# Kernel tuning notes

Hardware: AMD Instinct MI355X
Metric: run time of the kernel (lower is better)

The kernel has to match this reference:

```python
import jax, jax.numpy as jnp
import numpy as np

B, D, C = 8192, 2048, 1000

def setup_inputs() -> dict:
    key = jax.random.key(0)
    k1, k2, k3 = jax.random.split(key, 3)
    x = jax.random.normal(k1, (B, D), dtype=jnp.float32)
    W = jax.random.normal(k2, (D, C), dtype=jnp.float32) * (1.0 / np.sqrt(D))
    b = jax.random.normal(k3, (C,), dtype=jnp.float32) * 0.01
    return {"x": x, "W": W, "b": b}

def reference(x, W, b):
    # inner classifier: logits out[b, c]
    out = jnp.dot(x, W) + b  # [B, C]
    # leave-one-out logsumexp per class, fused:
    # lse_k = logsumexp(out[:, != k]) = lse_all + log1p(-exp(out_k - lse_all))
    lse = jax.nn.logsumexp(out, axis=1, keepdims=True)  # [B, 1]
    loo = lse + jnp.log1p(-jnp.exp(out - lse))           # [B, C]
    # c_out = -loo; return c_out + out
    return out - loo
```

## Files before the change

### kernel.cpp

```cpp
#include <hip/hip_runtime.h>
#include <hip/hip_bf16.h>
#include <math.h>

#define BDIM 8192
#define DDIM 2048
#define CDIM 1000
#define NPAD 1024
#define BK   64

#define WS_BT_OFFSET  33554432ULL
#define WS_P0_OFFSET  37748736ULL
#define WS_P1_OFFSET  54132736ULL
#define WS_NEED       70516736ULL

typedef __attribute__((ext_vector_type(8))) short short8;
typedef __attribute__((ext_vector_type(4))) float floatx4;

__device__ __forceinline__ unsigned short f2bf(float f) {
    union { float f; unsigned u; } a; a.f = f;
    unsigned u = a.u;
    u = (u + 0x7fff + ((u >> 16) & 1)) >> 16;
    return (unsigned short)u;
}

__device__ __forceinline__ float bf2f(unsigned short h) {
    union { unsigned u; float f; } a; a.u = ((unsigned)h) << 16;
    return a.f;
}

__device__ __forceinline__ void async_copy16(const void* gp, void* lp) {
    __builtin_amdgcn_global_load_lds(
        (const __attribute__((address_space(1))) void*)gp,
        (__attribute__((address_space(3))) void*)lp,
        16, 0, 0);
}

__global__ __launch_bounds__(256) void cvt_kernel(
    const float* __restrict__ x, unsigned short* __restrict__ xb,
    const float* __restrict__ W, unsigned short* __restrict__ Bt)
{
    const int blk = blockIdx.x;
    const int t   = threadIdx.x;
    if (blk < 16384) {
        int i = blk * 256 + t;
        float4 v = ((const float4*)x)[i];
        ushort4 o;
        o.x = f2bf(v.x); o.y = f2bf(v.y); o.z = f2bf(v.z); o.w = f2bf(v.w);
        ((ushort4*)xb)[i] = o;
    } else {
        __shared__ float tile[32][33];
        const int b2 = blk - 16384;
        const int k0 = (b2 & 63) * 32;
        const int n0 = (b2 >> 6) * 32;
        const int tx = t & 31, ty = t >> 5;
        #pragma unroll
        for (int i = 0; i < 4; i++) {
            int k = k0 + ty + i * 8;
            int n = n0 + tx;
            tile[ty + i * 8][tx] = (n < CDIM) ? W[(size_t)k * CDIM + n] : 0.0f;
        }
        __syncthreads();
        #pragma unroll
        for (int i = 0; i < 4; i++) {
            int n = n0 + ty + i * 8;
            int k = k0 + tx;
            Bt[(size_t)n * DDIM + k] = f2bf(tile[tx][ty + i * 8]);
        }
    }
}

template <bool BF16OUT>
__device__ __forceinline__ void gemm_body(
    const unsigned short* __restrict__ A,
    const unsigned short* __restrict__ Bt,
    void* __restrict__ Cv,
    int mBase, int nBase, int kBase, int kIters,
    unsigned short* As, unsigned short* Bs)
{
    const int t    = threadIdx.x;
    const int wave = t >> 6;
    const int lane = t & 63;
    const int wm   = wave & 1;
    const int wn   = wave >> 1;
    const int quad = lane >> 4;
    const int l16  = lane & 15;

    floatx4 acc[4][4] = {};

    const int rowA = t >> 3;
    const int csw  = ((t & 7) ^ (rowA & 7)) * 16;
    const char* Ag = (const char*)A  + ((size_t)(mBase + rowA) * DDIM + kBase) * 2 + csw;
    const char* Bg = (const char*)Bt + ((size_t)(nBase + rowA) * DDIM + kBase) * 2 + csw;
    char* AsDst = (char*)As + t * 16;
    char* BsDst = (char*)Bs + t * 16;

    const int xorb0 = ((0 * 4 + quad) ^ (l16 & 7)) * 8;
    const int xorb1 = ((1 * 4 + quad) ^ (l16 & 7)) * 8;

    for (int kt = 0; kt < kIters * BK; kt += BK) {
        const char* a = Ag + kt * 2;
        const char* b = Bg + kt * 2;
        #pragma unroll
        for (int r = 0; r < 4; r++) {
            async_copy16(a + (size_t)r * 32 * DDIM * 2, AsDst + r * 4096);
            async_copy16(b + (size_t)r * 32 * DDIM * 2, BsDst + r * 4096);
        }
        __syncthreads();

        #pragma unroll
        for (int ks = 0; ks < 2; ks++) {
            const int xorb = ks ? xorb1 : xorb0;
            short8 af[4], bfr[4];
            #pragma unroll
            for (int mi = 0; mi < 4; mi++)
                af[mi] = *(const short8*)(As + (wm * 64 + mi * 16 + l16) * BK + xorb);
            #pragma unroll
            for (int ni = 0; ni < 4; ni++)
                bfr[ni] = *(const short8*)(Bs + (wn * 64 + ni * 16 + l16) * BK + xorb);
            #pragma unroll
            for (int mi = 0; mi < 4; mi++)
                #pragma unroll
                for (int ni = 0; ni < 4; ni++)
                    acc[mi][ni] = __builtin_amdgcn_mfma_f32_16x16x32_bf16(
                        af[mi], bfr[ni], acc[mi][ni], 0, 0, 0);
        }
        __syncthreads();
    }

    #pragma unroll
    for (int mi = 0; mi < 4; mi++) {
        int row0 = mBase + wm * 64 + mi * 16 + quad * 4;
        #pragma unroll
        for (int ni = 0; ni < 4; ni++) {
            int col = nBase + wn * 64 + ni * 16 + l16;
            if (col < CDIM) {
                #pragma unroll
                for (int rg = 0; rg < 4; rg++) {
                    if (BF16OUT)
                        ((unsigned short*)Cv)[(size_t)(row0 + rg) * CDIM + col] =
                            f2bf(acc[mi][ni][rg]);
                    else
                        ((float*)Cv)[(size_t)(row0 + rg) * CDIM + col] = acc[mi][ni][rg];
                }
            }
        }
    }
}

__global__ __launch_bounds__(256, 2) void gemm_single_kernel(
    const unsigned short* __restrict__ A,
    const unsigned short* __restrict__ Bt,
    float* __restrict__ C0)
{
    __shared__ unsigned short As[128 * BK];
    __shared__ unsigned short Bs[128 * BK];

    const int L   = blockIdx.x;
    const int xcd = L & 7;
    const int s   = L >> 3;
    const int m_t = xcd * 8 + (s >> 3);
    const int n_t = s & 7;

    gemm_body<false>(A, Bt, C0, m_t * 128, n_t * 128, 0, DDIM / BK, As, Bs);
}


#define STAGE_A(BUF, EXT, KO)                                                 \
    do {                                                                      \
        _Pragma("unroll")                                                     \
        for (int h = 0; h < 2; h++) {                                         \
            const int row_ = rA0 + (EXT) + h * 128;                           \
            async_copy16(gA + (size_t)row_ * DDIM + (KO),                     \
                         &As[BUF][row_ * BK + c8]);                           \
        }                                                                     \
    } while (0)

#define STAGE_B(BUF, EXT, KO)                                                 \
    do {                                                                      \
        _Pragma("unroll")                                                     \
        for (int h = 0; h < 2; h++) {                                         \
            const int row_ = rB0 + (EXT) + h * 128;                           \
            async_copy16(gB + (size_t)row_ * DDIM + (KO),                     \
                         &Bs[BUF][row_ * BK + c8]);                           \
        }                                                                     \
    } while (0)

#define LOADA(BUF, MQ)                                                        \
    do {                                                                      \
        _Pragma("unroll")                                                     \
        for (int mf = 0; mf < 4; mf++) {                                      \
            const int r_ = (arA + (MQ) * 64 + mf * 16) * BK;                  \
            af[mf][0] = *(const short8*)&As[BUF][r_ + xorb0];                 \
            af[mf][1] = *(const short8*)&As[BUF][r_ + xorb1];                 \
        }                                                                     \
    } while (0)

#define LOADB(BUF, NQ, BF)                                                    \
    do {                                                                      \
        _Pragma("unroll")                                                     \
        for (int nf = 0; nf < 2; nf++) {                                      \
            const int r_ = (arB + (NQ) * 32 + nf * 16) * BK;                  \
            BF[nf][0] = *(const short8*)&Bs[BUF][r_ + xorb0];                 \
            BF[nf][1] = *(const short8*)&Bs[BUF][r_ + xorb1];                 \
        }                                                                     \
    } while (0)

#define MMAC(MQ, NQ, BF)                                                      \
    do {                                                                      \
        __builtin_amdgcn_s_setprio(1);                                        \
        _Pragma("unroll")                                                     \
        for (int mf = 0; mf < 4; mf++) {                                      \
            _Pragma("unroll")                                                 \
            for (int nf = 0; nf < 2; nf++) {                                  \
                floatx4 c_ = acc[(MQ) * 4 + mf][(NQ) * 2 + nf];               \
                c_ = __builtin_amdgcn_mfma_f32_16x16x32_bf16(                 \
                    af[mf][0], BF[nf][0], c_, 0, 0, 0);                       \
                c_ = __builtin_amdgcn_mfma_f32_16x16x32_bf16(                 \
                    af[mf][1], BF[nf][1], c_, 0, 0, 0);                       \
                acc[(MQ) * 4 + mf][(NQ) * 2 + nf] = c_;                       \
            }                                                                 \
        }                                                                     \
        __builtin_amdgcn_s_setprio(0);                                        \
    } while (0)

#define RAW_BARRIER() asm volatile("s_barrier" ::: "memory")

__global__ __launch_bounds__(512) void gemm8_kernel(
    const unsigned short* __restrict__ A,
    const unsigned short* __restrict__ Bt,
    unsigned short* __restrict__ P0, unsigned short* __restrict__ P1)
{
    __shared__ unsigned short As[2][256 * BK];
    __shared__ unsigned short Bs[2][256 * BK];

    const int t    = threadIdx.x;
    const int wave = t >> 6;
    const int lane = t & 63;
    const int wm   = wave >> 2;
    const int wn   = wave & 3;
    const int quad = lane >> 4;
    const int l16  = lane & 15;

    const int L    = blockIdx.x;
    const int g    = (L & 7) * 32 + (L >> 3);
    const int z    = g & 1;
    const int tid2 = g >> 1;
    const int mBase = (tid2 >> 2) * 256;
    const int nBase = (tid2 & 3) * 256;
    const int kBase = z * (DDIM / 2);
    const int NTt   = (DDIM / 2) / BK;

    const int c8  = (t & 7) << 3;
    const int q0  = t >> 3;
    const int csw = (((t & 7) ^ (q0 & 7)) << 3);
    const int rA0 = q0;
    const int rB0 = q0 + (q0 & 32);
    const unsigned short* gA = A  + (size_t)mBase * DDIM + kBase + csw;
    const unsigned short* gB = Bt + (size_t)nBase * DDIM + kBase + csw;

    const int xorb0 = ((0 * 4 + quad) ^ (l16 & 7)) << 3;
    const int xorb1 = ((1 * 4 + quad) ^ (l16 & 7)) << 3;
    const int arA = wm * 128 + l16;
    const int arB = wn * 64 + l16;

    floatx4 acc[8][4] = {};
    short8 af[4][2], bf0[2][2], bf1[2][2];

    STAGE_A(0, 0, 0);
    STAGE_A(0, 64, 0);
    STAGE_B(0, 0, 0);
    STAGE_B(0, 32, 0);
    STAGE_A(1, 0, BK);
    STAGE_B(1, 0, BK);
    STAGE_B(1, 32, BK);
    asm volatile("s_waitcnt vmcnt(6)" ::: "memory");
    RAW_BARRIER();

    for (int j = 0; j < NTt; j++) {
        const int buf = j & 1;
        const int ko1 = (j + 1) * BK;
        const int ko2 = (j + 2) * BK;
        const bool s1 = (j + 1 < NTt);
        const bool s2 = (j + 2 < NTt);

        if (buf == 0) { LOADA(0, 0); LOADB(0, 0, bf0); }
        else          { LOADA(1, 0); LOADB(1, 0, bf0); }
        if (s1) { if (buf == 0) STAGE_A(1, 64, ko1); else STAGE_A(0, 64, ko1); }
        RAW_BARRIER();
        MMAC(0, 0, bf0);
        RAW_BARRIER();

        if (buf == 0) LOADB(0, 1, bf1); else LOADB(1, 1, bf1);
        if (s2) { if (buf == 0) STAGE_A(0, 0, ko2); else STAGE_A(1, 0, ko2); }
        RAW_BARRIER();
        MMAC(0, 1, bf1);
        RAW_BARRIER();

        if (buf == 0) LOADA(0, 1); else LOADA(1, 1);
        if (s2) { if (buf == 0) STAGE_B(0, 0, ko2); else STAGE_B(1, 0, ko2); }
        RAW_BARRIER();
        MMAC(1, 0, bf0);
        RAW_BARRIER();

        if (s2) { if (buf == 0) STAGE_B(0, 32, ko2); else STAGE_B(1, 32, ko2); }
        if (j < NTt - 3) asm volatile("s_waitcnt vmcnt(6)" ::: "memory");
        else             asm volatile("s_waitcnt vmcnt(0)" ::: "memory");
        RAW_BARRIER();
        MMAC(1, 1, bf1);
        RAW_BARRIER();
    }

    unsigned short* P = z ? P1 : P0;
    #pragma unroll
    for (int mfg = 0; mfg < 8; mfg++) {
        const int row0 = mBase + wm * 128 + mfg * 16 + quad * 4;
        #pragma unroll
        for (int nfg = 0; nfg < 4; nfg++) {
            const int col = nBase + wn * 64 + nfg * 16 + l16;
            if (col < CDIM) {
                #pragma unroll
                for (int rg = 0; rg < 4; rg++)
                    P[(size_t)(row0 + rg) * CDIM + col] = f2bf(acc[mfg][nfg][rg]);
            }
        }
    }
}

__global__ __launch_bounds__(256) void lse_kernel(
    float* __restrict__ out,
    const unsigned short* P0, const unsigned short* P1,
    const float* __restrict__ bias, int split)
{
    const int row = blockIdx.x;
    const int t   = threadIdx.x;
    __shared__ float red[8];

    const bool valid = t < (CDIM / 4);
    const int c0 = t * 4;

    float4 v = make_float4(-INFINITY, -INFINITY, -INFINITY, -INFINITY);
    float4 e = make_float4(0.f, 0.f, 0.f, 0.f);
    if (valid) {
        if (split) {
            ushort4 p0 = *(const ushort4*)(P0 + (size_t)row * CDIM + c0);
            ushort4 p1 = *(const ushort4*)(P1 + (size_t)row * CDIM + c0);
            v.x = bf2f(p0.x) + bf2f(p1.x);
            v.y = bf2f(p0.y) + bf2f(p1.y);
            v.z = bf2f(p0.z) + bf2f(p1.z);
            v.w = bf2f(p0.w) + bf2f(p1.w);
        } else {
            v = *(const float4*)(out + (size_t)row * CDIM + c0);
        }
        float4 bb = *(const float4*)(bias + c0);
        v.x += bb.x; v.y += bb.y; v.z += bb.z; v.w += bb.w;
    }

    float m = fmaxf(fmaxf(v.x, v.y), fmaxf(v.z, v.w));
    #pragma unroll
    for (int off = 32; off > 0; off >>= 1)
        m = fmaxf(m, __shfl_down(m, off, 64));
    const int wave = t >> 6;
    if ((t & 63) == 0) red[wave] = m;
    __syncthreads();
    if (t == 0) red[4] = fmaxf(fmaxf(red[0], red[1]), fmaxf(red[2], red[3]));
    __syncthreads();
    const float M = red[4];

    float s = 0.f;
    if (valid) {
        e.x = expf(v.x - M); e.y = expf(v.y - M);
        e.z = expf(v.z - M); e.w = expf(v.w - M);
        s = e.x + e.y + e.z + e.w;
    }
    #pragma unroll
    for (int off = 32; off > 0; off >>= 1)
        s += __shfl_down(s, off, 64);
    if ((t & 63) == 0) red[wave] = s;
    __syncthreads();
    if (t == 0) red[4] = red[0] + red[1] + red[2] + red[3];
    __syncthreads();
    const float S    = red[4];
    const float lse  = M + logf(S);
    const float invS = 1.0f / S;

    if (valid) {
        float4 o;
        o.x = (v.x - lse) - log1pf(-e.x * invS);
        o.y = (v.y - lse) - log1pf(-e.y * invS);
        o.z = (v.z - lse) - log1pf(-e.z * invS);
        o.w = (v.w - lse) - log1pf(-e.w * invS);
        *(float4*)(out + (size_t)row * CDIM + c0) = o;
    }
}

extern "C" void kernel_launch(void* const* d_in, const int* in_sizes, int n_in,
                              void* d_out, int out_size, void* d_ws, size_t ws_size,
                              hipStream_t stream) {
    const float* x = (const float*)d_in[0];
    const float* W = (const float*)d_in[1];
    const float* b = (const float*)d_in[2];
    float* out = (float*)d_out;

    unsigned short* xb = (unsigned short*)d_ws;
    unsigned short* Bt = (unsigned short*)((char*)d_ws + WS_BT_OFFSET);
    unsigned short* P0 = (unsigned short*)((char*)d_ws + WS_P0_OFFSET);
    unsigned short* P1 = (unsigned short*)((char*)d_ws + WS_P1_OFFSET);
    const bool splitk = ws_size >= WS_NEED;

    cvt_kernel<<<18432, 256, 0, stream>>>(x, xb, W, Bt);

    if (splitk) {
        gemm8_kernel<<<256, 512, 0, stream>>>(xb, Bt, P0, P1);
        lse_kernel<<<BDIM, 256, 0, stream>>>(out, P0, P1, b, 1);
    } else {
        gemm_single_kernel<<<512, 256, 0, stream>>>(xb, Bt, out);
        lse_kernel<<<BDIM, 256, 0, stream>>>(out, nullptr, nullptr, b, 0);
    }
}
```

Baseline: 178.1 us.

## Deepen GEMM prefetch, coarsen convert kernel, use one wave per row in LSE

Three separate changes. The conversion kernel now has each block convert eight float4 chunks of x, so far fewer blocks are launched. The GEMM main loop now issues all of a stage's A and B loads two tiles ahead, with a deeper vmcnt wait, so global loads have more time to complete. The LSE kernel assigns one wave per row and reduces with xor shuffles only, which removes the shared memory and __syncthreads steps, at the cost of fewer threads per row.

```diff
diff --git a/kernel.cpp b/kernel.cpp
--- a/kernel.cpp
+++ b/kernel.cpp
@@ -41,15 +41,19 @@
 {
     const int blk = blockIdx.x;
     const int t   = threadIdx.x;
-    if (blk < 16384) {
+    if (blk < 2048) {
         int i = blk * 256 + t;
-        float4 v = ((const float4*)x)[i];
-        ushort4 o;
-        o.x = f2bf(v.x); o.y = f2bf(v.y); o.z = f2bf(v.z); o.w = f2bf(v.w);
-        ((ushort4*)xb)[i] = o;
+        #pragma unroll
+        for (int it = 0; it < 8; it++) {
+            float4 v = ((const float4*)x)[i];
+            ushort4 o;
+            o.x = f2bf(v.x); o.y = f2bf(v.y); o.z = f2bf(v.z); o.w = f2bf(v.w);
+            ((ushort4*)xb)[i] = o;
+            i += 2048 * 256;
+        }
     } else {
         __shared__ float tile[32][33];
-        const int b2 = blk - 16384;
+        const int b2 = blk - 2048;
         const int k0 = (b2 & 63) * 32;
         const int n0 = (b2 >> 6) * 32;
         const int tx = t & 31, ty = t >> 5;
@@ -271,39 +275,40 @@
     STAGE_B(0, 0, 0);
     STAGE_B(0, 32, 0);
     STAGE_A(1, 0, BK);
+    STAGE_A(1, 64, BK);
     STAGE_B(1, 0, BK);
     STAGE_B(1, 32, BK);
-    asm volatile("s_waitcnt vmcnt(6)" ::: "memory");
+    asm volatile("s_waitcnt vmcnt(8)" ::: "memory");
     RAW_BARRIER();
 
     for (int j = 0; j < NTt; j++) {
         const int buf = j & 1;
-        const int ko1 = (j + 1) * BK;
         const int ko2 = (j + 2) * BK;
-        const bool s1 = (j + 1 < NTt);
         const bool s2 = (j + 2 < NTt);
 
         if (buf == 0) { LOADA(0, 0); LOADB(0, 0, bf0); }
         else          { LOADA(1, 0); LOADB(1, 0, bf0); }
-        if (s1) { if (buf == 0) STAGE_A(1, 64, ko1); else STAGE_A(0, 64, ko1); }
         RAW_BARRIER();
         MMAC(0, 0, bf0);
         RAW_BARRIER();
 
         if (buf == 0) LOADB(0, 1, bf1); else LOADB(1, 1, bf1);
-        if (s2) { if (buf == 0) STAGE_A(0, 0, ko2); else STAGE_A(1, 0, ko2); }
+        if (s2) {
+            if (buf == 0) { STAGE_A(0, 0, ko2); STAGE_B(0, 0, ko2); }
+            else          { STAGE_A(1, 0, ko2); STAGE_B(1, 0, ko2); }
+        }
         RAW_BARRIER();
         MMAC(0, 1, bf1);
         RAW_BARRIER();
 
         if (buf == 0) LOADA(0, 1); else LOADA(1, 1);
-        if (s2) { if (buf == 0) STAGE_B(0, 0, ko2); else STAGE_B(1, 0, ko2); }
+        if (s2) { if (buf == 0) STAGE_B(0, 32, ko2); else STAGE_B(1, 32, ko2); }
         RAW_BARRIER();
         MMAC(1, 0, bf0);
         RAW_BARRIER();
 
-        if (s2) { if (buf == 0) STAGE_B(0, 32, ko2); else STAGE_B(1, 32, ko2); }
-        if (j < NTt - 3) asm volatile("s_waitcnt vmcnt(6)" ::: "memory");
+        if (s2) { if (buf == 0) STAGE_A(0, 64, ko2); else STAGE_A(1, 64, ko2); }
+        if (j < NTt - 2) asm volatile("s_waitcnt vmcnt(8)" ::: "memory");
         else             asm volatile("s_waitcnt vmcnt(0)" ::: "memory");
         RAW_BARRIER();
         MMAC(1, 1, bf1);
@@ -331,65 +336,75 @@
     const unsigned short* P0, const unsigned short* P1,
     const float* __restrict__ bias, int split)
 {
-    const int row = blockIdx.x;
-    const int t   = threadIdx.x;
-    __shared__ float red[8];
-
-    const bool valid = t < (CDIM / 4);
-    const int c0 = t * 4;
-
-    float4 v = make_float4(-INFINITY, -INFINITY, -INFINITY, -INFINITY);
-    float4 e = make_float4(0.f, 0.f, 0.f, 0.f);
-    if (valid) {
-        if (split) {
-            ushort4 p0 = *(const ushort4*)(P0 + (size_t)row * CDIM + c0);
-            ushort4 p1 = *(const ushort4*)(P1 + (size_t)row * CDIM + c0);
-            v.x = bf2f(p0.x) + bf2f(p1.x);
-            v.y = bf2f(p0.y) + bf2f(p1.y);
-            v.z = bf2f(p0.z) + bf2f(p1.z);
-            v.w = bf2f(p0.w) + bf2f(p1.w);
+    const int wave = threadIdx.x >> 6;
+    const int lane = threadIdx.x & 63;
+    const int row  = blockIdx.x * 4 + wave;
+    const int cb   = lane * 16;
+
+    float4 v[4], e[4];
+    #pragma unroll
+    for (int q = 0; q < 4; q++) {
+        const int c0 = cb + q * 4;
+        if (c0 < CDIM) {
+            float4 vv;
+            if (split) {
+                ushort4 p0 = *(const ushort4*)(P0 + (size_t)row * CDIM + c0);
+                ushort4 p1 = *(const ushort4*)(P1 + (size_t)row * CDIM + c0);
+                vv.x = bf2f(p0.x) + bf2f(p1.x);
+                vv.y = bf2f(p0.y) + bf2f(p1.y);
+                vv.z = bf2f(p0.z) + bf2f(p1.z);
+                vv.w = bf2f(p0.w) + bf2f(p1.w);
+            } else {
+                vv = *(const float4*)(out + (size_t)row * CDIM + c0);
+            }
+            float4 bb = *(const float4*)(bias + c0);
+            vv.x += bb.x; vv.y += bb.y; vv.z += bb.z; vv.w += bb.w;
+            v[q] = vv;
         } else {
-            v = *(const float4*)(out + (size_t)row * CDIM + c0);
-        }
-        float4 bb = *(const float4*)(bias + c0);
-        v.x += bb.x; v.y += bb.y; v.z += bb.z; v.w += bb.w;
-    }
-
-    float m = fmaxf(fmaxf(v.x, v.y), fmaxf(v.z, v.w));
-    #pragma unroll
-    for (int off = 32; off > 0; off >>= 1)
-        m = fmaxf(m, __shfl_down(m, off, 64));
-    const int wave = t >> 6;
-    if ((t & 63) == 0) red[wave] = m;
-    __syncthreads();
-    if (t == 0) red[4] = fmaxf(fmaxf(red[0], red[1]), fmaxf(red[2], red[3]));
-    __syncthreads();
-    const float M = red[4];
+            v[q] = make_float4(-INFINITY, -INFINITY, -INFINITY, -INFINITY);
+        }
+    }
+
+    float m = -INFINITY;
+    #pragma unroll
+    for (int q = 0; q < 4; q++)
+        m = fmaxf(m, fmaxf(fmaxf(v[q].x, v[q].y), fmaxf(v[q].z, v[q].w)));
+    #pragma unroll
+    for (int off = 1; off < 64; off <<= 1)
+        m = fmaxf(m, __shfl_xor(m, off, 64));
+    const float M = m;
 
     float s = 0.f;
-    if (valid) {
-        e.x = expf(v.x - M); e.y = expf(v.y - M);
-        e.z = expf(v.z - M); e.w = expf(v.w - M);
-        s = e.x + e.y + e.z + e.w;
-    }
-    #pragma unroll
-    for (int off = 32; off > 0; off >>= 1)
-        s += __shfl_down(s, off, 64);
-    if ((t & 63) == 0) red[wave] = s;
-    __syncthreads();
-    if (t == 0) red[4] = red[0] + red[1] + red[2] + red[3];
-    __syncthreads();
-    const float S    = red[4];
+    #pragma unroll
+    for (int q = 0; q < 4; q++) {
+        const int c0 = cb + q * 4;
+        if (c0 < CDIM) {
+            e[q].x = expf(v[q].x - M); e[q].y = expf(v[q].y - M);
+            e[q].z = expf(v[q].z - M); e[q].w = expf(v[q].w - M);
+            s += e[q].x + e[q].y + e[q].z + e[q].w;
+        } else {
+            e[q] = make_float4(0.f, 0.f, 0.f, 0.f);
+        }
+    }
+    #pragma unroll
+    for (int off = 1; off < 64; off <<= 1)
+        s += __shfl_xor(s, off, 64);
+
+    const float S    = s;
     const float lse  = M + logf(S);
     const float invS = 1.0f / S;
 
-    if (valid) {
-        float4 o;
-        o.x = (v.x - lse) - log1pf(-e.x * invS);
-        o.y = (v.y - lse) - log1pf(-e.y * invS);
-        o.z = (v.z - lse) - log1pf(-e.z * invS);
-        o.w = (v.w - lse) - log1pf(-e.w * invS);
-        *(float4*)(out + (size_t)row * CDIM + c0) = o;
+    #pragma unroll
+    for (int q = 0; q < 4; q++) {
+        const int c0 = cb + q * 4;
+        if (c0 < CDIM) {
+            float4 o;
+            o.x = (v[q].x - lse) - log1pf(-e[q].x * invS);
+            o.y = (v[q].y - lse) - log1pf(-e[q].y * invS);
+            o.z = (v[q].z - lse) - log1pf(-e[q].z * invS);
+            o.w = (v[q].w - lse) - log1pf(-e[q].w * invS);
+            *(float4*)(out + (size_t)row * CDIM + c0) = o;
+        }
     }
 }
 
@@ -407,13 +422,13 @@
     unsigned short* P1 = (unsigned short*)((char*)d_ws + WS_P1_OFFSET);
     const bool splitk = ws_size >= WS_NEED;
 
-    cvt_kernel<<<18432, 256, 0, stream>>>(x, xb, W, Bt);
+    cvt_kernel<<<4096, 256, 0, stream>>>(x, xb, W, Bt);
 
     if (splitk) {
         gemm8_kernel<<<256, 512, 0, stream>>>(xb, Bt, P0, P1);
-        lse_kernel<<<BDIM, 256, 0, stream>>>(out, P0, P1, b, 1);
+        lse_kernel<<<2048, 256, 0, stream>>>(out, P0, P1, b, 1);
     } else {
         gemm_single_kernel<<<512, 256, 0, stream>>>(xb, Bt, out);
-        lse_kernel<<<BDIM, 256, 0, stream>>>(out, nullptr, nullptr, b, 0);
-    }
-}
+        lse_kernel<<<2048, 256, 0, stream>>>(out, nullptr, nullptr, b, 0);
+    }
+}
```

New measurement: 184.7 us. 1.04x slower.
